# Optimization experiments

Hardware: AMD Instinct MI355X
Metric: run time of the kernel (lower is better)

The kernel has to match this reference:

```python
import jax, jax.numpy as jnp
import numpy as np

IN = (8, 8, 8, 8)
OUT = (8, 8, 8, 8)
RANK = (1, 16, 16, 16, 1)  # boundary ranks = 1
BATCH = 4096


def setup_inputs() -> dict:
    key = jax.random.key(0)
    ks = jax.random.split(key, 5)
    x = jax.random.normal(ks[0], (BATCH, int(np.prod(IN))), dtype=jnp.float32)
    scale = 0.7  # matches nn.init.uniform_(f, -0.7, 0.7)
    factors = {}
    for k in range(4):
        shp = (RANK[k], OUT[k], IN[k], RANK[k + 1])
        factors[f"f{k}"] = jax.random.uniform(ks[k + 1], shp, jnp.float32, -scale, scale)
    bias = jnp.zeros((int(np.prod(OUT)),), dtype=jnp.float32)  # init.constant_(bias, 0)
    return {"x": x, **factors, "bias": bias}


def reference(x, f0, f1, f2, f3, bias):
    """TT-matrix linear: y = TT(W) @ x_vec + bias, cores of shape (r1, o, i, r2)."""
    cores = [f0, f1, f2, f3]
    B = x.shape[0]
    i0 = cores[0].shape[2]
    # t: (B, A=accumulated out dims, r=current rank, i=current in dim, X=remaining in dims)
    t = x.reshape(B, 1, 1, i0, -1)
    n = len(cores)
    for k, c in enumerate(cores):
        r1, o, i, r2 = c.shape
        # contract current rank and current input mode
        t = jnp.einsum('barix,rois->baosx', t, c)
        A = t.shape[1] * t.shape[2]
        X = t.shape[4]
        if k + 1 < n:
            i_next = cores[k + 1].shape[2]
            t = t.reshape(B, A, r2, i_next, X // i_next)
        else:
            t = t.reshape(B, A)  # r2 == 1, X == 1
    return t + bias
```

## Files before the change

kernel.cpp:

```cpp
#include <hip/hip_runtime.h>

typedef unsigned short u16;
typedef unsigned int u32;
typedef __attribute__((ext_vector_type(8))) short bf16x8;
typedef __attribute__((ext_vector_type(4))) float f32x4;

__device__ __forceinline__ u16 f2bf(float f) {
  u32 u = __float_as_uint(f);
  u += 0x7fffu + ((u >> 16) & 1u);
  return (u16)(u >> 16);
}

__global__ void prep_small(const float* __restrict__ f0, const float* __restrict__ f1,
                           const float* __restrict__ f2, const float* __restrict__ f3,
                           float* __restrict__ W01, float* __restrict__ W23) {
  int b = blockIdx.x;
  if (b < 256) {
    int idx = b * 256 + threadIdx.x;
    int r2 = idx & 15; int t = idx >> 4;
    int i1 = t & 7; t >>= 3;
    int i0 = t & 7; t >>= 3;
    int o1 = t & 7; int o0 = t >> 3;
    const float* a = f0 + (o0 * 8 + i0) * 16;
    const float* c = f1 + (o1 * 8 + i1) * 16 + r2;
    float s = 0.f;
#pragma unroll
    for (int r1 = 0; r1 < 16; ++r1) s += a[r1] * c[r1 * 1024];
    W01[idx] = s;
  } else {
    int idx = (b - 256) * 256 + threadIdx.x;
    int i3 = idx & 7, o3 = (idx >> 3) & 7, i2 = (idx >> 6) & 7;
    int o2 = (idx >> 9) & 7, r2 = idx >> 12;
    const float* a = f2 + ((r2 * 8 + o2) * 8 + i2) * 16;
    const float* c = f3 + o3 * 8 + i3;
    float s = 0.f;
#pragma unroll
    for (int r3 = 0; r3 < 16; ++r3) s += a[r3] * c[r3 * 64];
    W23[idx] = s;
  }
}

__global__ void prep_big(const float* __restrict__ W01, const float* __restrict__ W23,
                         const float* __restrict__ x, u16* __restrict__ W,
                         uint4* __restrict__ xb) {
  int b = blockIdx.x;
  if (b < 8192) {
    int idx = b * 256 + threadIdx.x;
    float4 a = ((const float4*)x)[idx * 2], d = ((const float4*)x)[idx * 2 + 1];
    union { u16 h[8]; uint4 v; } r;
    r.h[0] = f2bf(a.x); r.h[1] = f2bf(a.y); r.h[2] = f2bf(a.z); r.h[3] = f2bf(a.w);
    r.h[4] = f2bf(d.x); r.h[5] = f2bf(d.y); r.h[6] = f2bf(d.z); r.h[7] = f2bf(d.w);
    xb[idx] = r.v;
    return;
  }
  const int o = b - 8192;
  const int o2 = (o >> 3) & 7, o3 = o & 7;
  const int tid = threadIdx.x;
  __shared__ float sW23[1024];
  {
    int e = tid * 4;
    const float* src = W23 + (e >> 6) * 4096 + o2 * 512 + ((e >> 3) & 7) * 64
                         + o3 * 8 + (e & 7);
    ((float4*)sW23)[tid] = *(const float4*)src;
  }
  float w01r[16];
  {
    const float* a = W01 + (((o >> 6) * 64 + (tid >> 2)) << 4);
#pragma unroll
    for (int q = 0; q < 4; ++q) {
      float4 v = *(const float4*)(a + q * 4);
      w01r[q * 4] = v.x; w01r[q * 4 + 1] = v.y; w01r[q * 4 + 2] = v.z; w01r[q * 4 + 3] = v.w;
    }
  }
  __syncthreads();

  const int i2a = 2 * (tid & 3), i2b = i2a + 1;
  float acc[16] = {};
#pragma unroll
  for (int r2 = 0; r2 < 16; ++r2) {
    const float w = w01r[r2];
    const float4 va0 = *(const float4*)(sW23 + r2 * 64 + i2a * 8);
    const float4 va1 = *(const float4*)(sW23 + r2 * 64 + i2a * 8 + 4);
    const float4 vb0 = *(const float4*)(sW23 + r2 * 64 + i2b * 8);
    const float4 vb1 = *(const float4*)(sW23 + r2 * 64 + i2b * 8 + 4);
    acc[0]  += w * va0.x; acc[1]  += w * va0.y; acc[2]  += w * va0.z; acc[3]  += w * va0.w;
    acc[4]  += w * va1.x; acc[5]  += w * va1.y; acc[6]  += w * va1.z; acc[7]  += w * va1.w;
    acc[8]  += w * vb0.x; acc[9]  += w * vb0.y; acc[10] += w * vb0.z; acc[11] += w * vb0.w;
    acc[12] += w * vb1.x; acc[13] += w * vb1.y; acc[14] += w * vb1.z; acc[15] += w * vb1.w;
  }
  union { u16 h[8]; uint4 v; } r0, r1;
#pragma unroll
  for (int j = 0; j < 8; ++j) { r0.h[j] = f2bf(acc[j]); r1.h[j] = f2bf(acc[8 + j]); }
  uint4* dst = (uint4*)(W + (size_t)o * 4096 + tid * 16);
  dst[0] = r0.v; dst[1] = r1.v;
}

__device__ __forceinline__ void gload_lds16(const void* g, void* l) {
  __builtin_amdgcn_global_load_lds((__attribute__((address_space(1))) void*)(g),
                                   (__attribute__((address_space(3))) void*)(l),
                                   16, 0, 0);
}

__global__ __launch_bounds__(512, 2) void gemm256(
    const u16* __restrict__ A, const u16* __restrict__ B,
    const float* __restrict__ bias, float* __restrict__ C) {
  constexpr int K = 4096, N = 4096, NT = 128;
  __shared__ u16 S[65536];
  const int tid  = threadIdx.x;
  const int wave = tid >> 6, lane = tid & 63;
  const int l15 = lane & 15, l4 = lane >> 4;
  const int wr = wave >> 2, wc = wave & 3;
  const int bm = (int)(blockIdx.x >> 4) * 256;
  const int bn = (int)(blockIdx.x & 15) * 256;

  const int rl = tid >> 2;
  const int ls = (tid & 3) ^ ((rl >> 1) & 3);
  const u16* srcA0 = A + (size_t)(bm +       rl) * K + ls * 8;
  const u16* srcA1 = A + (size_t)(bm + 128 + rl) * K + ls * 8;
  const u16* srcB0 = B + (size_t)(bn +       rl) * K + ls * 8;
  const u16* srcB1 = B + (size_t)(bn + 128 + rl) * K + ls * 8;
  const int dA0 = wave * 512,         dA1 = 4096  + wave * 512;
  const int dB0 = 8192 + wave * 512,  dB1 = 12288 + wave * 512;

  int offA[8], offB[4];
#pragma unroll
  for (int mi = 0; mi < 8; ++mi) {
    int r = wr * 128 + mi * 16 + l15;
    offA[mi] = r * 32 + ((l4 ^ ((r >> 1) & 3)) * 8);
  }
#pragma unroll
  for (int ni = 0; ni < 4; ++ni) {
    int r = wc * 64 + ni * 16 + l15;
    offB[ni] = 8192 + r * 32 + ((l4 ^ ((r >> 1) & 3)) * 8);
  }

#define STAGE_A(kts) do { int _s = (kts) & 3; u16* _b = S + _s * 16384;          \
    gload_lds16(srcA0 + (size_t)(kts) * 32, _b + dA0);                           \
    gload_lds16(srcA1 + (size_t)(kts) * 32, _b + dA1); } while (0)
#define STAGE_B(kts) do { int _s = (kts) & 3; u16* _b = S + _s * 16384;          \
    gload_lds16(srcB0 + (size_t)(kts) * 32, _b + dB0);                           \
    gload_lds16(srcB1 + (size_t)(kts) * 32, _b + dB1); } while (0)

#define ITER(kt, bvU, bvL)                                                       \
  {                                                                              \
    const u16* base  = S + ((kt) & 3) * 16384;                                   \
    const u16* baseN = S + (((kt) + 1) & 3) * 16384;                             \
    const int kn = ((kt) + 3) & (NT - 1);                                        \
        \
    bf16x8 avN[4];                                                               \
    _Pragma("unroll")                                                            \
    for (int i = 0; i < 4; ++i) avN[i] = *(const bf16x8*)(base + offA[4 + i]);   \
    STAGE_A(kn);                                                                 \
    __builtin_amdgcn_s_setprio(1);                                               \
    _Pragma("unroll")                                                            \
    for (int mi = 0; mi < 4; ++mi)                                               \
      _Pragma("unroll")                                                          \
      for (int ni = 0; ni < 4; ++ni)                                             \
        acc[mi][ni] = __builtin_amdgcn_mfma_f32_16x16x32_bf16(                   \
            avC[mi], bvU[ni], acc[mi][ni], 0, 0, 0);                             \
    __builtin_amdgcn_s_setprio(0);                                               \
      \
    STAGE_B(kn);                                                                 \
    asm volatile("s_waitcnt vmcnt(8)" ::: "memory");                             \
    __builtin_amdgcn_sched_barrier(0);                                           \
    __builtin_amdgcn_s_barrier();                                                \
    _Pragma("unroll")                                                            \
    for (int i = 0; i < 4; ++i) avC[i] = *(const bf16x8*)(baseN + offA[i]);      \
    _Pragma("unroll")                                                            \
    for (int i = 0; i < 4; ++i) bvL[i] = *(const bf16x8*)(baseN + offB[i]);      \
    __builtin_amdgcn_s_setprio(1);                                               \
    _Pragma("unroll")                                                            \
    for (int mi = 0; mi < 4; ++mi)                                               \
      _Pragma("unroll")                                                          \
      for (int ni = 0; ni < 4; ++ni)                                             \
        acc[4 + mi][ni] = __builtin_amdgcn_mfma_f32_16x16x32_bf16(               \
            avN[mi], bvU[ni], acc[4 + mi][ni], 0, 0, 0);                         \
    __builtin_amdgcn_s_setprio(0);                                               \
    __builtin_amdgcn_s_barrier();                                                \
  }

  STAGE_A(0); STAGE_B(0);
  STAGE_A(1); STAGE_B(1);
  STAGE_A(2); STAGE_B(2);
  asm volatile("s_waitcnt vmcnt(8)" ::: "memory");
  __builtin_amdgcn_sched_barrier(0);
  __builtin_amdgcn_s_barrier();

  f32x4 acc[8][4] = {};
  bf16x8 avC[4], bvE[4], bvO[4];
#pragma unroll
  for (int i = 0; i < 4; ++i) avC[i] = *(const bf16x8*)(S + offA[i]);
#pragma unroll
  for (int i = 0; i < 4; ++i) bvE[i] = *(const bf16x8*)(S + offB[i]);

  for (int kt = 0; kt < NT; kt += 2) {
    ITER(kt,     bvE, bvO)
    ITER(kt + 1, bvO, bvE)
  }

#pragma unroll
  for (int ni = 0; ni < 4; ++ni) {
    const int col = bn + wc * 64 + ni * 16 + l15;
    const float bvs = bias[col];
#pragma unroll
    for (int mi = 0; mi < 8; ++mi) {
      const int row0 = bm + wr * 128 + mi * 16 + l4 * 4;
#pragma unroll
      for (int j = 0; j < 4; ++j)
        C[(size_t)(row0 + j) * N + col] = acc[mi][ni][j] + bvs;
    }
  }
  asm volatile("s_waitcnt vmcnt(0)" ::: "memory");
#undef STAGE_A
#undef STAGE_B
#undef ITER
}

extern "C" void kernel_launch(void* const* d_in, const int* in_sizes, int n_in,
                              void* d_out, int out_size, void* d_ws, size_t ws_size,
                              hipStream_t stream) {
  const float* x    = (const float*)d_in[0];
  const float* f0   = (const float*)d_in[1];
  const float* f1   = (const float*)d_in[2];
  const float* f2   = (const float*)d_in[3];
  const float* f3   = (const float*)d_in[4];
  const float* bias = (const float*)d_in[5];

  char* ws = (char*)d_ws;
  u16* Wb = (u16*)(ws);
  u16* xb = (u16*)(ws + 33554432);
  float* W01 = (float*)d_out;
  float* W23 = (float*)d_out + 65536;

  prep_small<<<512,   256, 0, stream>>>(f0, f1, f2, f3, W01, W23);
  prep_big  <<<12288, 256, 0, stream>>>(W01, W23, x, Wb, (uint4*)xb);
  gemm256   <<<256,   512, 0, stream>>>(xb, Wb, bias, (float*)d_out);
}
```

Before: 148.6 us.

## Ping-pong wave groups between LDS reads and MFMA phases in GEMM main loop

Restructures the GEMM inner loop so the two wave-rows alternate roles: while one half of the block issues LDS fragment reads, the other half runs MFMAs, separated by block barriers each phase. This replaces the previous per-wave software pipelining with register double-buffered fragments (avC/avN, bvE/bvO). The intent is to overlap LDS traffic and matrix math across waves and to reduce register pressure. In exchange it adds four barriers per k-tile, and the role split between the halves relies on matching barrier counts.

```diff
diff --git a/kernel.cpp b/kernel.cpp
--- a/kernel.cpp
+++ b/kernel.cpp
@@ -110,6 +110,7 @@
   const int wave = tid >> 6, lane = tid & 63;
   const int l15 = lane & 15, l4 = lane >> 4;
   const int wr = wave >> 2, wc = wave & 3;
+  const bool isL = (wr == 0);
   const int bm = (int)(blockIdx.x >> 4) * 256;
   const int bn = (int)(blockIdx.x & 15) * 256;
 
@@ -141,43 +142,36 @@
     gload_lds16(srcB0 + (size_t)(kts) * 32, _b + dB0);                           \
     gload_lds16(srcB1 + (size_t)(kts) * 32, _b + dB1); } while (0)
 
-#define ITER(kt, bvU, bvL)                                                       \
-  {                                                                              \
-    const u16* base  = S + ((kt) & 3) * 16384;                                   \
-    const u16* baseN = S + (((kt) + 1) & 3) * 16384;                             \
-    const int kn = ((kt) + 3) & (NT - 1);                                        \
-        \
-    bf16x8 avN[4];                                                               \
-    _Pragma("unroll")                                                            \
-    for (int i = 0; i < 4; ++i) avN[i] = *(const bf16x8*)(base + offA[4 + i]);   \
-    STAGE_A(kn);                                                                 \
+#define READ_U0(base_) do {                                                      \
+    _Pragma("unroll")                                                            \
+    for (int i = 0; i < 4; ++i) av0[i] = *(const bf16x8*)((base_) + offA[i]);    \
+    _Pragma("unroll")                                                            \
+    for (int i = 0; i < 4; ++i) bv[i]  = *(const bf16x8*)((base_) + offB[i]);    \
+  } while (0)
+#define READ_U1(base_) do {                                                      \
+    _Pragma("unroll")                                                            \
+    for (int i = 0; i < 4; ++i) av1[i] = *(const bf16x8*)((base_) + offA[4 + i]);\
+  } while (0)
+#define MFMA_U0() do {                                                           \
     __builtin_amdgcn_s_setprio(1);                                               \
     _Pragma("unroll")                                                            \
     for (int mi = 0; mi < 4; ++mi)                                               \
       _Pragma("unroll")                                                          \
       for (int ni = 0; ni < 4; ++ni)                                             \
         acc[mi][ni] = __builtin_amdgcn_mfma_f32_16x16x32_bf16(                   \
-            avC[mi], bvU[ni], acc[mi][ni], 0, 0, 0);                             \
+            av0[mi], bv[ni], acc[mi][ni], 0, 0, 0);                              \
     __builtin_amdgcn_s_setprio(0);                                               \
-      \
-    STAGE_B(kn);                                                                 \
-    asm volatile("s_waitcnt vmcnt(8)" ::: "memory");                             \
-    __builtin_amdgcn_sched_barrier(0);                                           \
-    __builtin_amdgcn_s_barrier();                                                \
-    _Pragma("unroll")                                                            \
-    for (int i = 0; i < 4; ++i) avC[i] = *(const bf16x8*)(baseN + offA[i]);      \
-    _Pragma("unroll")                                                            \
-    for (int i = 0; i < 4; ++i) bvL[i] = *(const bf16x8*)(baseN + offB[i]);      \
+  } while (0)
+#define MFMA_U1() do {                                                           \
     __builtin_amdgcn_s_setprio(1);                                               \
     _Pragma("unroll")                                                            \
     for (int mi = 0; mi < 4; ++mi)                                               \
       _Pragma("unroll")                                                          \
       for (int ni = 0; ni < 4; ++ni)                                             \
         acc[4 + mi][ni] = __builtin_amdgcn_mfma_f32_16x16x32_bf16(               \
-            avN[mi], bvU[ni], acc[4 + mi][ni], 0, 0, 0);                         \
+            av1[mi], bv[ni], acc[4 + mi][ni], 0, 0, 0);                          \
     __builtin_amdgcn_s_setprio(0);                                               \
-    __builtin_amdgcn_s_barrier();                                                \
-  }
+  } while (0)
 
   STAGE_A(0); STAGE_B(0);
   STAGE_A(1); STAGE_B(1);
@@ -187,16 +181,33 @@
   __builtin_amdgcn_s_barrier();
 
   f32x4 acc[8][4] = {};
-  bf16x8 avC[4], bvE[4], bvO[4];
-#pragma unroll
-  for (int i = 0; i < 4; ++i) avC[i] = *(const bf16x8*)(S + offA[i]);
-#pragma unroll
-  for (int i = 0; i < 4; ++i) bvE[i] = *(const bf16x8*)(S + offB[i]);
-
-  for (int kt = 0; kt < NT; kt += 2) {
-    ITER(kt,     bvE, bvO)
-    ITER(kt + 1, bvO, bvE)
-  }
+  bf16x8 av0[4], av1[4], bv[4];
+
+  for (int kt = 0; kt < NT; ++kt) {
+    const u16* base = S + (kt & 3) * 16384;
+    const int kn = (kt + 3) & (NT - 1);
+
+    if (isL)          READ_U0(base);
+    else if (kt > 0)  MFMA_U1();
+    STAGE_A(kn);
+    __builtin_amdgcn_s_barrier();
+
+    if (isL)  MFMA_U0();
+    else      READ_U0(base);
+    __builtin_amdgcn_s_barrier();
+
+    if (isL)  READ_U1(base);
+    else      MFMA_U0();
+    STAGE_B(kn);
+    __builtin_amdgcn_s_barrier();
+
+    if (isL)  MFMA_U1();
+    else      READ_U1(base);
+    asm volatile("s_waitcnt vmcnt(8)" ::: "memory");
+    __builtin_amdgcn_sched_barrier(0);
+    __builtin_amdgcn_s_barrier();
+  }
+  if (!isL) MFMA_U1();
 
 #pragma unroll
   for (int ni = 0; ni < 4; ++ni) {
@@ -213,7 +224,10 @@
   asm volatile("s_waitcnt vmcnt(0)" ::: "memory");
 #undef STAGE_A
 #undef STAGE_B
-#undef ITER
+#undef READ_U0
+#undef READ_U1
+#undef MFMA_U0
+#undef MFMA_U1
 }
 
 extern "C" void kernel_launch(void* const* d_in, const int* in_sizes, int n_in,
```

Result: slower. 152.7 us (+2.8%).
